# Kernel tuning notes

Measured on AMD Instinct MI355X. Metric: run time of the kernel, lower is better.

## Reference

```python
import jax, jax.numpy as jnp
import numpy as np

VOCAB = 32000
HIDDEN = 512
B, T = 8, 512
LN_EPS = 1e-5


def setup_inputs() -> dict:
    key = jax.random.key(0)
    ks = jax.random.split(key, 9)
    s = 0.02
    return {
        "input_ids": jax.random.randint(ks[0], (B, T), 0, VOCAB),
        "emb": jax.random.normal(ks[1], (VOCAB, HIDDEN), jnp.float32) * s,
        "w_ih": jax.random.normal(ks[2], (3 * HIDDEN, HIDDEN), jnp.float32) * s,
        "w_hh": jax.random.normal(ks[3], (3 * HIDDEN, HIDDEN), jnp.float32) * s,
        "b_ih": jnp.zeros((3 * HIDDEN,), jnp.float32),
        "b_hh": jnp.zeros((3 * HIDDEN,), jnp.float32),
        "ln_gamma": jnp.ones((HIDDEN,), jnp.float32),
        "ln_beta": jnp.zeros((HIDDEN,), jnp.float32),
        "head_w": jax.random.normal(ks[4], (VOCAB, HIDDEN), jnp.float32) * s,
        "head_b": jnp.zeros((VOCAB,), jnp.float32),
    }


def _gru_scan(xg, w_hh, b_hh):
    # xg: [T, B, 3H]  (input-side gate pre-activations, PyTorch gate order r,z,n)
    H = xg.shape[-1] // 3
    h0 = jnp.zeros((xg.shape[1], H), xg.dtype)

    def step(h, xg_t):
        hg = h @ w_hh.T + b_hh              # [B, 3H]
        xr, xz, xn = jnp.split(xg_t, 3, axis=-1)
        hr, hz, hn = jnp.split(hg, 3, axis=-1)
        r = jax.nn.sigmoid(xr + hr)
        z = jax.nn.sigmoid(xz + hz)
        n = jnp.tanh(xn + r * hn)
        h_new = (1.0 - z) * n + z * h
        return h_new, h_new

    _, hs = jax.lax.scan(step, h0, xg)
    return hs  # [T, B, H]


def reference(input_ids, emb, w_ih, w_hh, b_ih, b_hh, ln_gamma, ln_beta, head_w, head_b):
    # embedding lookup: [B, T, H]
    x = emb[input_ids]
    # precompute input-side gate pre-activations for all timesteps: [B, T, 3H]
    xg = jnp.einsum("bth,gh->btg", x, w_ih) + b_ih
    # sequential GRU over time
    hs = _gru_scan(jnp.swapaxes(xg, 0, 1), w_hh, b_hh)  # [T, B, H]
    hs = jnp.swapaxes(hs, 0, 1)                          # [B, T, H]
    # LayerNorm over hidden dim
    mu = jnp.mean(hs, axis=-1, keepdims=True)
    var = jnp.mean(jnp.square(hs - mu), axis=-1, keepdims=True)
    y = (hs - mu) * jax.lax.rsqrt(var + LN_EPS) * ln_gamma + ln_beta
    # output head: [B, T, V]
    logits = jnp.einsum("bth,vh->btv", y, head_w) + head_b
    return logits
```

## Files before the change

### kernel.cpp

```cpp
#include <hip/hip_runtime.h>
#include <hip/hip_bf16.h>
#include <stdint.h>

#define VOCAB 32000
#define HID 512
#define NB 8
#define SEQ 512
#define NG 1536
#define LN_EPS 1e-5f
#define GRU_WGS 32
#define GRU_SPIN_BUDGET (1 << 20)

typedef short bf16x8 __attribute__((ext_vector_type(8)));
typedef float f32x4 __attribute__((ext_vector_type(4)));

__device__ __forceinline__ unsigned short f2bf(float f) {
  union { float f; uint32_t u; } c; c.f = f;
  return (unsigned short)((c.u + 0x7fffu + ((c.u >> 16) & 1u)) >> 16);
}

__global__ void init_ws_kernel(uint32_t* h_state) {
  int i = blockIdx.x * 256 + threadIdx.x;
  if (i < 8 * HID) h_state[i] = 0u;
  else if (i < 16 * HID) h_state[i] = 0x00010001u;
}

__global__ void conv_bf16_kernel(const float* __restrict__ in,
                                 unsigned short* __restrict__ out, int n4) {
  int i = blockIdx.x * 256 + threadIdx.x;
  if (i >= n4) return;
  const float4 v = ((const float4*)in)[i];
  ushort4 o;
  o.x = f2bf(v.x); o.y = f2bf(v.y); o.z = f2bf(v.z); o.w = f2bf(v.w);
  ((ushort4*)out)[i] = o;
}

__global__ void embed_kernel(const int* __restrict__ ids,
                             const float* __restrict__ emb,
                             unsigned short* __restrict__ out) {
  int row = blockIdx.x;
  int id = ids[row];
  int c = threadIdx.x * 2;
  const float2 v = *(const float2*)(emb + (size_t)id * HID + c);
  ushort2 o; o.x = f2bf(v.x); o.y = f2bf(v.y);
  *(ushort2*)(out + (size_t)row * HID + c) = o;
}

#define BM 128
#define BN 128
#define BK 32

__global__ __launch_bounds__(256, 2) void gemm_bt_kernel(
    const unsigned short* __restrict__ A, const unsigned short* __restrict__ B,
    const float* __restrict__ bias, float* __restrict__ C, int N, int nbn) {
  __shared__ unsigned short a_lds[BM * BK];
  __shared__ unsigned short b_lds[BN * BK];
  const int nwg = gridDim.x;
  const int chunk = nwg >> 3;
  const int bid = blockIdx.x;
  const int sw = (bid & 7) * chunk + (bid >> 3);
  const int bm = sw / nbn, bn = sw % nbn;
  const int tid = threadIdx.x;
  const int lane = tid & 63, wid = tid >> 6;
  const int wm = wid >> 1, wn = wid & 1;

  f32x4 acc[4][4] = {};

  for (int kt = 0; kt < HID / BK; ++kt) {
    __syncthreads();
#pragma unroll
    for (int p = 0; p < 2; ++p) {
      const int flat = (p * 256 + tid) * 16;
      const int row = flat >> 6;
      const int kb = flat & 63;
      const char* ga =
          (const char*)(A + ((size_t)(bm * BM + row) * HID + kt * BK)) + kb;
      const char* gb =
          (const char*)(B + ((size_t)(bn * BN + row) * HID + kt * BK)) + kb;
      char* la = (char*)a_lds + (size_t)(p * 256 + wid * 64) * 16;
      char* lb = (char*)b_lds + (size_t)(p * 256 + wid * 64) * 16;
      __builtin_amdgcn_global_load_lds(
          (const __attribute__((address_space(1))) void*)ga,
          (__attribute__((address_space(3))) void*)la, 16, 0, 0);
      __builtin_amdgcn_global_load_lds(
          (const __attribute__((address_space(1))) void*)gb,
          (__attribute__((address_space(3))) void*)lb, 16, 0, 0);
    }
    __syncthreads();
    bf16x8 af[4], bfr[4];
#pragma unroll
    for (int i = 0; i < 4; ++i) {
      af[i] = *(const bf16x8*)(a_lds + (wm * 64 + i * 16 + (lane & 15)) * BK +
                               (lane >> 4) * 8);
      bfr[i] = *(const bf16x8*)(b_lds + (wn * 64 + i * 16 + (lane & 15)) * BK +
                                (lane >> 4) * 8);
    }
#pragma unroll
    for (int i = 0; i < 4; ++i)
#pragma unroll
      for (int j = 0; j < 4; ++j)
        acc[i][j] =
            __builtin_amdgcn_mfma_f32_16x16x32_bf16(af[i], bfr[j], acc[i][j], 0, 0, 0);
  }
#pragma unroll
  for (int i = 0; i < 4; ++i) {
    const int mrow = bm * BM + wm * 64 + i * 16 + (lane >> 4) * 4;
#pragma unroll
    for (int j = 0; j < 4; ++j) {
      const int col = bn * BN + wn * 64 + j * 16 + (lane & 15);
      const float bv = bias[col];
#pragma unroll
      for (int r = 0; r < 4; ++r)
        C[(size_t)(mrow + r) * N + col] = acc[i][j][r] + bv;
    }
  }
}

__global__ __launch_bounds__(64, 1) void gru_kernel(
    const float* __restrict__ xg, const float* __restrict__ w_hh,
    const float* __restrict__ b_hh, float* __restrict__ hs,
    unsigned short* h_state) {
  const int wid = blockIdx.x;
  const int lane = threadIdx.x;
  const int col16 = lane & 15;
  const int kq = lane >> 4;

  __shared__ float h_pub[8][16];

  bf16x8 wf[3][16];
#pragma unroll
  for (int g = 0; g < 3; ++g) {
    const float* wr =
        w_hh + (size_t)(g * HID + wid * 16 + col16) * HID + kq * 8;
#pragma unroll
    for (int kk = 0; kk < 16; ++kk) {
      float4 f0 = *(const float4*)(wr + kk * 32);
      float4 f1 = *(const float4*)(wr + kk * 32 + 4);
      bf16x8 v;
      v[0] = (short)f2bf(f0.x); v[1] = (short)f2bf(f0.y);
      v[2] = (short)f2bf(f0.z); v[3] = (short)f2bf(f0.w);
      v[4] = (short)f2bf(f1.x); v[5] = (short)f2bf(f1.y);
      v[6] = (short)f2bf(f1.z); v[7] = (short)f2bf(f1.w);
      wf[g][kk] = v;
    }
  }
  const float bh_r = b_hh[0 * HID + wid * 16 + col16];
  const float bh_z = b_hh[1 * HID + wid * 16 + col16];
  const float bh_n = b_hh[2 * HID + wid * 16 + col16];

  const int abase = col16 * HID + kq * 8;
  const bool realrow = col16 < 8;
  const bool owner = lane < 32;
  const int bbase = kq * 4;

  float xr[4], xz[4], xn[4];
#pragma unroll
  for (int r = 0; r < 4; ++r) { xr[r] = 0.f; xz[r] = 0.f; xn[r] = 0.f; }
  if (owner) {
#pragma unroll
    for (int r = 0; r < 4; ++r) {
      const size_t xo = (size_t)(bbase + r) * SEQ * NG + wid * 16 + col16;
      xr[r] = xg[xo];
      xz[r] = xg[xo + HID];
      xn[r] = xg[xo + 2 * HID];
    }
  }
  float hprev[4] = {0.f, 0.f, 0.f, 0.f};
  int budget = GRU_SPIN_BUDGET;

  for (int t = 0; t < SEQ; ++t) {
    const unsigned short* rd = h_state + (size_t)(t & 1) * (16 * HID);
    unsigned short* wpub = h_state + (size_t)((t + 1) & 1) * (16 * HID);
    const uint32_t texp = (uint32_t)((t >> 1) & 1);
    const uint32_t tpub = (uint32_t)(((t + 1) >> 1) & 1);

    uint64_t hb[32];
#pragma unroll
    for (int kk = 0; kk < 32; ++kk) hb[kk] = 0;
    {
      bool ok = false;
      while (!ok && budget > 0) {
        uint32_t bad = 0;
        if (realrow) {
#pragma unroll
          for (int kk = 0; kk < 16; ++kk) {
            const uint64_t* ap = (const uint64_t*)(rd + abase + kk * 32);
            hb[2 * kk] = __hip_atomic_load(ap, __ATOMIC_RELAXED,
                                           __HIP_MEMORY_SCOPE_AGENT);
            hb[2 * kk + 1] = __hip_atomic_load(ap + 1, __ATOMIC_RELAXED,
                                               __HIP_MEMORY_SCOPE_AGENT);
          }
#pragma unroll
          for (int kk = 0; kk < 32; ++kk) {
            bad |= (uint32_t)hb[kk] ^ texp;
            bad |= (uint32_t)(hb[kk] >> 32) ^ texp;
          }
          bad &= 1u;
        }
        ok = (__ballot(bad == 0u) == ~0ULL);
        --budget;
      }
    }

    float xrn[4], xzn[4], xnn[4];
#pragma unroll
    for (int r = 0; r < 4; ++r) { xrn[r] = 0.f; xzn[r] = 0.f; xnn[r] = 0.f; }
    if (owner && t + 1 < SEQ) {
#pragma unroll
      for (int r = 0; r < 4; ++r) {
        const size_t xo = (size_t)(bbase + r) * SEQ * NG +
                          (size_t)(t + 1) * NG + wid * 16 + col16;
        xrn[r] = xg[xo];
        xzn[r] = xg[xo + HID];
        xnn[r] = xg[xo + 2 * HID];
      }
    }

    f32x4 ar0 = {0.f, 0.f, 0.f, 0.f}, ar1 = {0.f, 0.f, 0.f, 0.f};
    f32x4 az0 = {0.f, 0.f, 0.f, 0.f}, az1 = {0.f, 0.f, 0.f, 0.f};
    f32x4 an0 = {0.f, 0.f, 0.f, 0.f}, an1 = {0.f, 0.f, 0.f, 0.f};
#pragma unroll
    for (int kk = 0; kk < 16; kk += 2) {
      union { uint64_t u[2]; bf16x8 v; } c0, c1;
      c0.u[0] = hb[2 * kk];     c0.u[1] = hb[2 * kk + 1];
      c1.u[0] = hb[2 * kk + 2]; c1.u[1] = hb[2 * kk + 3];
      ar0 = __builtin_amdgcn_mfma_f32_16x16x32_bf16(c0.v, wf[0][kk], ar0, 0, 0, 0);
      az0 = __builtin_amdgcn_mfma_f32_16x16x32_bf16(c0.v, wf[1][kk], az0, 0, 0, 0);
      an0 = __builtin_amdgcn_mfma_f32_16x16x32_bf16(c0.v, wf[2][kk], an0, 0, 0, 0);
      ar1 = __builtin_amdgcn_mfma_f32_16x16x32_bf16(c1.v, wf[0][kk + 1], ar1, 0, 0, 0);
      az1 = __builtin_amdgcn_mfma_f32_16x16x32_bf16(c1.v, wf[1][kk + 1], az1, 0, 0, 0);
      an1 = __builtin_amdgcn_mfma_f32_16x16x32_bf16(c1.v, wf[2][kk + 1], an1, 0, 0, 0);
    }
    const f32x4 ar = ar0 + ar1, az = az0 + az1, an = an0 + an1;

    float hnew[4] = {0.f, 0.f, 0.f, 0.f};
    if (owner) {
#pragma unroll
      for (int r = 0; r < 4; ++r) {
        const float rg = 1.f / (1.f + __expf(-(xr[r] + ar[r] + bh_r)));
        const float zg = 1.f / (1.f + __expf(-(xz[r] + az[r] + bh_z)));
        const float a = xn[r] + rg * (an[r] + bh_n);
        const float e2 = __expf(-2.f * fabsf(a));
        const float nn = copysignf((1.f - e2) / (1.f + e2), a);
        hnew[r] = (1.f - zg) * nn + zg * hprev[r];
        hprev[r] = hnew[r];
        h_pub[bbase + r][col16] = hnew[r];
      }
    }
    asm volatile("s_waitcnt lgkmcnt(0)" ::: "memory");
    __builtin_amdgcn_sched_barrier(0);
    if (lane < 32) {
      const int tb = lane >> 2;
      const int tq = (lane & 3) * 4;
      const float4 hp = *(const float4*)&h_pub[tb][tq];
      union { unsigned short s[4]; uint64_t u; } pk;
      pk.s[0] = (unsigned short)((f2bf(hp.x) & ~(unsigned short)1) | tpub);
      pk.s[1] = f2bf(hp.y);
      pk.s[2] = (unsigned short)((f2bf(hp.z) & ~(unsigned short)1) | tpub);
      pk.s[3] = f2bf(hp.w);
      uint64_t* dst = (uint64_t*)(wpub + tb * HID + wid * 16 + tq);
      __hip_atomic_store(dst, pk.u, __ATOMIC_RELAXED,
                         __HIP_MEMORY_SCOPE_AGENT);
    }
    if (owner) {
#pragma unroll
      for (int r = 0; r < 4; ++r)
        hs[((size_t)(bbase + r) * SEQ + t) * HID + wid * 16 + col16] = hnew[r];
    }
#pragma unroll
    for (int r = 0; r < 4; ++r) { xr[r] = xrn[r]; xz[r] = xzn[r]; xn[r] = xnn[r]; }
  }
}

__global__ __launch_bounds__(256) void ln_kernel(
    const float* __restrict__ hs, const float* __restrict__ gamma,
    const float* __restrict__ beta, unsigned short* __restrict__ y) {
  const int row = blockIdx.x * 4 + (threadIdx.x >> 6);
  const int lane = threadIdx.x & 63;
  const float* x = hs + (size_t)row * HID + lane * 8;
  float v[8];
  *(float4*)v = *(const float4*)x;
  *(float4*)(v + 4) = *(const float4*)(x + 4);
  float s = 0.f, q = 0.f;
#pragma unroll
  for (int j = 0; j < 8; ++j) { s += v[j]; q += v[j] * v[j]; }
#pragma unroll
  for (int off = 32; off > 0; off >>= 1) {
    s += __shfl_xor(s, off);
    q += __shfl_xor(q, off);
  }
  const float mu = s * (1.f / 512.f);
  const float is = rsqrtf(q * (1.f / 512.f) - mu * mu + LN_EPS);
  const float* gp = gamma + lane * 8;
  const float* bp = beta + lane * 8;
  union { unsigned short o[8]; uint4 u; } pk;
#pragma unroll
  for (int j = 0; j < 8; ++j) pk.o[j] = f2bf((v[j] - mu) * is * gp[j] + bp[j]);
  *(uint4*)(y + (size_t)row * HID + lane * 8) = pk.u;
}

extern "C" void kernel_launch(void* const* d_in, const int* in_sizes, int n_in,
                              void* d_out, int out_size, void* d_ws,
                              size_t ws_size, hipStream_t stream) {
  const int* ids = (const int*)d_in[0];
  const float* emb = (const float*)d_in[1];
  const float* w_ih = (const float*)d_in[2];
  const float* w_hh = (const float*)d_in[3];
  const float* b_ih = (const float*)d_in[4];
  const float* b_hh = (const float*)d_in[5];
  const float* gamma = (const float*)d_in[6];
  const float* beta = (const float*)d_in[7];
  const float* head_w = (const float*)d_in[8];
  const float* head_b = (const float*)d_in[9];
  float* out = (float*)d_out;

  char* ws = (char*)d_ws;
  size_t off = 0;
  auto alloc = [&](size_t bytes) -> void* {
    void* p = ws + off;
    off = (off + bytes + 255) & ~(size_t)255;
    return p;
  };
  unsigned short* h_state = (unsigned short*)alloc(2 * 16 * HID * 2);
  unsigned short* A1 = (unsigned short*)alloc((size_t)NB * SEQ * HID * 2);
  unsigned short* wihb = (unsigned short*)alloc((size_t)NG * HID * 2);
  unsigned short* hwb = (unsigned short*)alloc((size_t)VOCAB * HID * 2);
  float* xg = (float*)alloc((size_t)NB * SEQ * NG * 4);
  float* hsb = (float*)alloc((size_t)NB * SEQ * HID * 4);
  unsigned short* yb = (unsigned short*)alloc((size_t)NB * SEQ * HID * 2);

  init_ws_kernel<<<32, 256, 0, stream>>>((uint32_t*)h_state);
  conv_bf16_kernel<<<(NG * HID / 4) / 256, 256, 0, stream>>>(w_ih, wihb,
                                                             NG * HID / 4);
  conv_bf16_kernel<<<(VOCAB * HID / 4) / 256, 256, 0, stream>>>(
      head_w, hwb, VOCAB * HID / 4);
  embed_kernel<<<NB * SEQ, 256, 0, stream>>>(ids, emb, A1);
  gemm_bt_kernel<<<(NB * SEQ / BM) * (NG / BN), 256, 0, stream>>>(
      A1, wihb, b_ih, xg, NG, NG / BN);
  gru_kernel<<<GRU_WGS, 64, 0, stream>>>(xg, w_hh, b_hh, hsb, h_state);
  ln_kernel<<<NB * SEQ / 4, 256, 0, stream>>>(hsb, gamma, beta, yb);
  gemm_bt_kernel<<<(NB * SEQ / BM) * (VOCAB / BN), 256, 0, stream>>>(
      yb, hwb, head_b, out, VOCAB, VOCAB / BN);
}
```

Baseline: 1.778 ms.

## Split GRU spin-wait into cheap sentinel poll plus selective stale-chunk reload

The per-step wait on the published hidden state now first polls one 64-bit word per lane until every producer's flag bits match. After that it loads the full 16 chunks and re-reads only the chunks still stale, instead of reloading all 32 words on every spin iteration. The xg prefetch moves to two steps ahead and is issued after the store, so its latency is off the critical spin/MFMA path. The risk is extra registers and an extra round of global latency per step from the two-phase poll.

```diff
diff --git a/kernel.cpp b/kernel.cpp
--- a/kernel.cpp
+++ b/kernel.cpp
@@ -116,10 +116,11 @@
   }
 }
 
-__global__ __launch_bounds__(64, 1) void gru_kernel(
-    const float* __restrict__ xg, const float* __restrict__ w_hh,
-    const float* __restrict__ b_hh, float* __restrict__ hs,
-    unsigned short* h_state) {
+__global__ __attribute__((amdgpu_flat_work_group_size(64, 64),
+                          amdgpu_waves_per_eu(1, 1)))
+void gru_kernel(const float* __restrict__ xg, const float* __restrict__ w_hh,
+                const float* __restrict__ b_hh, float* __restrict__ hs,
+                unsigned short* h_state) {
   const int wid = blockIdx.x;
   const int lane = threadIdx.x;
   const int col16 = lane & 15;
@@ -153,16 +154,19 @@
   const bool owner = lane < 32;
   const int bbase = kq * 4;
 
-  float xr[4], xz[4], xn[4];
-#pragma unroll
-  for (int r = 0; r < 4; ++r) { xr[r] = 0.f; xz[r] = 0.f; xn[r] = 0.f; }
+  float xc[12], xn_[12];
+#pragma unroll
+  for (int r = 0; r < 12; ++r) { xc[r] = 0.f; xn_[r] = 0.f; }
   if (owner) {
 #pragma unroll
     for (int r = 0; r < 4; ++r) {
       const size_t xo = (size_t)(bbase + r) * SEQ * NG + wid * 16 + col16;
-      xr[r] = xg[xo];
-      xz[r] = xg[xo + HID];
-      xn[r] = xg[xo + 2 * HID];
+      xc[r] = xg[xo];
+      xc[4 + r] = xg[xo + HID];
+      xc[8 + r] = xg[xo + 2 * HID];
+      xn_[r] = xg[xo + NG];
+      xn_[4 + r] = xg[xo + NG + HID];
+      xn_[8 + r] = xg[xo + NG + 2 * HID];
     }
   }
   float hprev[4] = {0.f, 0.f, 0.f, 0.f};
@@ -174,46 +178,54 @@
     const uint32_t texp = (uint32_t)((t >> 1) & 1);
     const uint32_t tpub = (uint32_t)(((t + 1) >> 1) & 1);
 
-    uint64_t hb[32];
-#pragma unroll
-    for (int kk = 0; kk < 32; ++kk) hb[kk] = 0;
     {
-      bool ok = false;
-      while (!ok && budget > 0) {
-        uint32_t bad = 0;
-        if (realrow) {
+      bool okl = true;
+      do {
+        if (lane < 32) {
+          const uint64_t* sp =
+              (const uint64_t*)(rd + (lane & 7) * HID + lane * 16);
+          const uint64_t s =
+              __hip_atomic_load(sp, __ATOMIC_RELAXED, __HIP_MEMORY_SCOPE_AGENT);
+          okl = ((((uint32_t)s ^ texp) | ((uint32_t)(s >> 32) ^ texp)) & 1u) ==
+                0u;
+        }
+      } while (__ballot(okl) != ~0ULL && --budget > 0);
+    }
+
+    uint4 hb[16];
+#pragma unroll
+    for (int kk = 0; kk < 16; ++kk) hb[kk] = make_uint4(0, 0, 0, 0);
+    {
+      uint32_t stale = realrow ? 0xFFFFu : 0u;
+      do {
+        if (stale) {
 #pragma unroll
           for (int kk = 0; kk < 16; ++kk) {
-            const uint64_t* ap = (const uint64_t*)(rd + abase + kk * 32);
-            hb[2 * kk] = __hip_atomic_load(ap, __ATOMIC_RELAXED,
+            if (stale & (1u << kk)) {
+              const uint4* ap = (const uint4*)(rd + abase + kk * 32);
+              hb[kk].x = __hip_atomic_load((const uint32_t*)ap + 0,
+                                           __ATOMIC_RELAXED,
                                            __HIP_MEMORY_SCOPE_AGENT);
-            hb[2 * kk + 1] = __hip_atomic_load(ap + 1, __ATOMIC_RELAXED,
-                                               __HIP_MEMORY_SCOPE_AGENT);
+              hb[kk].y = __hip_atomic_load((const uint32_t*)ap + 1,
+                                           __ATOMIC_RELAXED,
+                                           __HIP_MEMORY_SCOPE_AGENT);
+              hb[kk].z = __hip_atomic_load((const uint32_t*)ap + 2,
+                                           __ATOMIC_RELAXED,
+                                           __HIP_MEMORY_SCOPE_AGENT);
+              hb[kk].w = __hip_atomic_load((const uint32_t*)ap + 3,
+                                           __ATOMIC_RELAXED,
+                                           __HIP_MEMORY_SCOPE_AGENT);
+            }
           }
 #pragma unroll
-          for (int kk = 0; kk < 32; ++kk) {
-            bad |= (uint32_t)hb[kk] ^ texp;
-            bad |= (uint32_t)(hb[kk] >> 32) ^ texp;
+          for (int kk = 0; kk < 16; ++kk) {
+            const uint32_t bad = ((hb[kk].x ^ texp) | (hb[kk].y ^ texp) |
+                                  (hb[kk].z ^ texp) | (hb[kk].w ^ texp)) &
+                                 1u;
+            if (!bad) stale &= ~(1u << kk);
           }
-          bad &= 1u;
         }
-        ok = (__ballot(bad == 0u) == ~0ULL);
-        --budget;
-      }
-    }
-
-    float xrn[4], xzn[4], xnn[4];
-#pragma unroll
-    for (int r = 0; r < 4; ++r) { xrn[r] = 0.f; xzn[r] = 0.f; xnn[r] = 0.f; }
-    if (owner && t + 1 < SEQ) {
-#pragma unroll
-      for (int r = 0; r < 4; ++r) {
-        const size_t xo = (size_t)(bbase + r) * SEQ * NG +
-                          (size_t)(t + 1) * NG + wid * 16 + col16;
-        xrn[r] = xg[xo];
-        xzn[r] = xg[xo + HID];
-        xnn[r] = xg[xo + 2 * HID];
-      }
+      } while (__ballot(stale != 0u) != 0ULL && --budget > 0);
     }
 
     f32x4 ar0 = {0.f, 0.f, 0.f, 0.f}, ar1 = {0.f, 0.f, 0.f, 0.f};
@@ -221,9 +233,9 @@
     f32x4 an0 = {0.f, 0.f, 0.f, 0.f}, an1 = {0.f, 0.f, 0.f, 0.f};
 #pragma unroll
     for (int kk = 0; kk < 16; kk += 2) {
-      union { uint64_t u[2]; bf16x8 v; } c0, c1;
-      c0.u[0] = hb[2 * kk];     c0.u[1] = hb[2 * kk + 1];
-      c1.u[0] = hb[2 * kk + 2]; c1.u[1] = hb[2 * kk + 3];
+      union { uint4 u; bf16x8 v; } c0, c1;
+      c0.u = hb[kk];
+      c1.u = hb[kk + 1];
       ar0 = __builtin_amdgcn_mfma_f32_16x16x32_bf16(c0.v, wf[0][kk], ar0, 0, 0, 0);
       az0 = __builtin_amdgcn_mfma_f32_16x16x32_bf16(c0.v, wf[1][kk], az0, 0, 0, 0);
       an0 = __builtin_amdgcn_mfma_f32_16x16x32_bf16(c0.v, wf[2][kk], an0, 0, 0, 0);
@@ -237,9 +249,9 @@
     if (owner) {
 #pragma unroll
       for (int r = 0; r < 4; ++r) {
-        const float rg = 1.f / (1.f + __expf(-(xr[r] + ar[r] + bh_r)));
-        const float zg = 1.f / (1.f + __expf(-(xz[r] + az[r] + bh_z)));
-        const float a = xn[r] + rg * (an[r] + bh_n);
+        const float rg = 1.f / (1.f + __expf(-(xc[r] + ar[r] + bh_r)));
+        const float zg = 1.f / (1.f + __expf(-(xc[4 + r] + az[r] + bh_z)));
+        const float a = xc[8 + r] + rg * (an[r] + bh_n);
         const float e2 = __expf(-2.f * fabsf(a));
         const float nn = copysignf((1.f - e2) / (1.f + e2), a);
         hnew[r] = (1.f - zg) * nn + zg * hprev[r];
@@ -268,7 +280,17 @@
         hs[((size_t)(bbase + r) * SEQ + t) * HID + wid * 16 + col16] = hnew[r];
     }
 #pragma unroll
-    for (int r = 0; r < 4; ++r) { xr[r] = xrn[r]; xz[r] = xzn[r]; xn[r] = xnn[r]; }
+    for (int r = 0; r < 12; ++r) xc[r] = xn_[r];
+    if (owner && t + 2 < SEQ) {
+#pragma unroll
+      for (int r = 0; r < 4; ++r) {
+        const size_t xo = (size_t)(bbase + r) * SEQ * NG +
+                          (size_t)(t + 2) * NG + wid * 16 + col16;
+        xn_[r] = xg[xo];
+        xn_[4 + r] = xg[xo + HID];
+        xn_[8 + r] = xg[xo + 2 * HID];
+      }
+    }
   }
 }
 
```

Result: slower. 2.086 ms (+17.4%).
